# Kernel optimization log

Hardware: AMD Instinct MI355X
Metric: run time of the kernel (lower is better)

## Reference

```python
import jax, jax.numpy as jnp
import numpy as np

B, S_ENC, S_DEC = 4, 2048, 1024
ENC_DIM, DEC_DIM, H = 1024, 1024, 16
CROSS_DIM = max(ENC_DIM, DEC_DIM)
HEAD_DIM_DEC = DEC_DIM // H
SCALE = HEAD_DIM_DEC ** 0.5  # module divides by dec_scaling only


def _linear_params(key, d_in, d_out):
    kw, kb = jax.random.split(key)
    bound = 1.0 / np.sqrt(d_in)
    W = jax.random.uniform(kw, (d_in, d_out), jnp.float32, -bound, bound)
    b = jax.random.uniform(kb, (d_out,), jnp.float32, -bound, bound)
    return W, b


def setup_inputs() -> dict:
    key = jax.random.key(0)
    ks = jax.random.split(key, 7)
    enc = jax.random.normal(ks[0], (B, S_ENC, ENC_DIM), jnp.float32)
    dec = jax.random.normal(ks[1], (B, S_DEC, DEC_DIM), jnp.float32)
    enc_mask = jax.random.uniform(ks[2], (B, 1, 1, S_ENC)) < 0.1
    q_w, q_b = _linear_params(ks[3], DEC_DIM, CROSS_DIM)
    k_w, k_b = _linear_params(ks[4], ENC_DIM, CROSS_DIM)
    v_w, v_b = _linear_params(ks[5], ENC_DIM, DEC_DIM)
    o_w, o_b = _linear_params(ks[6], DEC_DIM, DEC_DIM)
    return {"enc": enc, "enc_mask": enc_mask, "dec": dec,
            "q_w": q_w, "q_b": q_b, "k_w": k_w, "k_b": k_b,
            "v_w": v_w, "v_b": v_b, "o_w": o_w, "o_b": o_b}


def _split_heads(x):
    b, s, d = x.shape
    return x.reshape(b, s, H, d // H).transpose(0, 2, 1, 3)  # [b,h,s,hd]


def reference(enc, enc_mask, dec, q_w, q_b, k_w, k_b, v_w, v_b, o_w, o_b):
    q = _split_heads(dec @ q_w + q_b)   # [B,H,Sq,cross_hd]
    k = _split_heads(enc @ k_w + k_b)   # [B,H,Sk,cross_hd]
    v = _split_heads(enc @ v_w + v_b)   # [B,H,Sk,dec_hd]
    logits = jnp.einsum('bhqd,bhkd->bhqk', q, k) / SCALE
    logits = jnp.where(enc_mask, -jnp.inf, logits)
    a = jax.nn.softmax(logits, axis=-1)
    x = jnp.einsum('bhqk,bhkd->bhqd', a, v)          # [B,H,Sq,dec_hd]
    x = x.transpose(0, 2, 1, 3).reshape(x.shape[0], x.shape[2], -1)  # [B,Sq,DEC_DIM]
    return x @ o_w + o_b
```

## Files before the change

kernel.cpp:

```cpp
#include <hip/hip_runtime.h>
#include <hip/hip_bf16.h>
#include <cstdint>

#define BB   4
#define SENC 2048
#define SDEC 1024
#define DM   1024
#define NH   16
#define HD   64

using short8 = __attribute__((ext_vector_type(8))) short;
using f32x4  = __attribute__((ext_vector_type(4))) float;

__device__ inline unsigned short f2bf(float f) {
    return (unsigned short)((__builtin_bit_cast(unsigned int, f) + 0x8000u) >> 16);
}
__device__ inline unsigned int pk2bf(float a, float b) {
    return ((__builtin_bit_cast(unsigned int, a) + 0x8000u) >> 16) |
           ((__builtin_bit_cast(unsigned int, b) + 0x8000u) & 0xffff0000u);
}

__device__ inline float fexp2(float x) {
#if __has_builtin(__builtin_amdgcn_exp2f)
    return __builtin_amdgcn_exp2f(x);
#else
    return exp2f(x);
#endif
}

#if __has_builtin(__builtin_amdgcn_global_load_lds)
#define HAS_GLL 1
#endif

__device__ inline void stage16(const void* g, void* l) {
#ifdef HAS_GLL
    typedef __attribute__((address_space(1))) const unsigned int guint;
    typedef __attribute__((address_space(3))) unsigned int luint;
    __builtin_amdgcn_global_load_lds((guint*)g, (luint*)l, 16, 0, 0);
#else
    *(short8*)l = *(const short8*)g;
#endif
}

__global__ __launch_bounds__(256) void prep_kernel(
    const float* __restrict__ dec, const float* __restrict__ enc,
    unsigned short* __restrict__ actb,
    const float* __restrict__ qw, const float* __restrict__ kw,
    const float* __restrict__ vw, const float* __restrict__ ow,
    unsigned short* __restrict__ qwt, unsigned short* __restrict__ kvwt,
    unsigned short* __restrict__ owt) {
    __shared__ float t[64][65];
    const int id = blockIdx.x, tid = threadIdx.x;
    if (id < 12288) {
        const int nd = BB * SDEC * DM;
        int i = (id * 256 + tid) * 4;
        const float* src = (i < nd) ? (dec + i) : (enc + (i - nd));
        float4 v = *(const float4*)src;
        ushort4 o;
        o.x = f2bf(v.x); o.y = f2bf(v.y); o.z = f2bf(v.z); o.w = f2bf(v.w);
        *(ushort4*)(actb + i) = o;
        return;
    }
    const int id2 = id - 12288;
    const int z = id2 >> 8, ky = (id2 >> 4) & 15, nx = id2 & 15;
    const float* src; unsigned short* dst;
    switch (z) {
        case 0:  src = qw; dst = qwt; break;
        case 1:  src = kw; dst = kvwt; break;
        case 2:  src = vw; dst = kvwt + (size_t)64 * 16384; break;
        default: src = ow; dst = owt; break;
    }
    const int k0 = ky * 64, n0 = nx * 64;
    #pragma unroll
    for (int it = 0; it < 16; ++it) {
        int e = it * 256 + tid, r = e >> 6, c = e & 63;
        t[r][c] = src[(size_t)(k0 + r) * DM + n0 + c];
    }
    __syncthreads();
    #pragma unroll
    for (int it = 0; it < 2; ++it) {
        int e = it * 256 + tid;
        int kg = e >> 6, r = e & 63;
        short8 w;
        #pragma unroll
        for (int j = 0; j < 8; ++j) w[j] = (short)f2bf(t[kg * 8 + j][r]);
        size_t off = (size_t)((n0 + r) >> 4) * 16384 + (size_t)((k0 >> 3) + kg) * 128
                   + ((r & 15) << 3);
        *(short8*)(dst + off) = w;
    }
}

__global__ __launch_bounds__(256) void gemm_qkv_kernel(
    const unsigned short* __restrict__ encb, const unsigned short* __restrict__ decb,
    const unsigned short* __restrict__ kvwt, const unsigned short* __restrict__ qwt,
    const float* __restrict__ q_b, const float* __restrict__ k_b, const float* __restrict__ v_b,
    unsigned short* __restrict__ Qb, unsigned short* __restrict__ Kb,
    unsigned short* __restrict__ Vtb) {
    __shared__ __align__(16) unsigned short As[2][128 * 32];
    const int id = blockIdx.x;
    const bool isKV = id < 1024;
    const unsigned short *A, *Bw;
    int m0, n0;
    if (isKV) {
        const int x = id & 7, w = id >> 3;
        A = encb; Bw = kvwt;
        m0 = (x * 8 + (w >> 4)) * 128;
        n0 = (w & 15) * 128;
    } else {
        const int i2 = id - 1024, x = i2 & 7, w = i2 >> 3;
        A = decb; Bw = qwt;
        m0 = (x * 4 + (w >> 3)) * 128;
        n0 = (w & 7) * 128;
    }
    const int tid = threadIdx.x;
    const int wave = tid >> 6, lane = tid & 63, quad = lane >> 4, l16 = lane & 15;
    const int wr = wave >> 1, wc = wave & 1;
    const int r16 = lane >> 2, c8 = (lane & 3) * 8;
    const int c8s = (((lane & 3) ^ ((r16 >> 1) & 3)) * 8);
    const int qsw8 = (quad ^ ((l16 >> 1) & 3)) * 8;
    f32x4 acc[4][4] = {};

    const unsigned short* Bbase = Bw + (size_t)(n0 >> 4) * 16384 + (size_t)(wc * 4) * 16384
                                + quad * 128 + l16 * 8;
    short8 bcur[4], bnxt[4];
    #pragma unroll
    for (int j = 0; j < 4; ++j) bcur[j] = *(const short8*)&Bbase[j * 16384];

    #pragma unroll
    for (int i = 0; i < 2; ++i) {
        const int row = wave * 32 + i * 16 + r16;
        stage16(&A[(size_t)(m0 + row) * DM + c8s], &As[0][row * 32 + c8]);
    }
    for (int it = 0; it < 32; ++it) {
        const int bf = it & 1;
        __syncthreads();
        if (it < 31) {
            const int kb2 = (it + 1) * 32, nb = bf ^ 1;
            #pragma unroll
            for (int i = 0; i < 2; ++i) {
                const int row = wave * 32 + i * 16 + r16;
                stage16(&A[(size_t)(m0 + row) * DM + kb2 + c8s], &As[nb][row * 32 + c8]);
            }
            #pragma unroll
            for (int j = 0; j < 4; ++j)
                bnxt[j] = *(const short8*)&Bbase[j * 16384 + kb2 * 16];
        }
        short8 af[4];
        #pragma unroll
        for (int i = 0; i < 4; ++i) af[i] = *(const short8*)&As[bf][(wr * 64 + i * 16 + l16) * 32 + qsw8];
        #pragma unroll
        for (int i = 0; i < 4; ++i)
            #pragma unroll
            for (int j = 0; j < 4; ++j)
                acc[i][j] = __builtin_amdgcn_mfma_f32_16x16x32_bf16(af[i], bcur[j], acc[i][j], 0, 0, 0);
        #pragma unroll
        for (int j = 0; j < 4; ++j) bcur[j] = bnxt[j];
    }
    #pragma unroll
    for (int i = 0; i < 4; ++i) {
        #pragma unroll
        for (int j = 0; j < 4; ++j) {
            const int gc = n0 + wc * 64 + j * 16 + l16;
            const int gr0 = m0 + wr * 64 + i * 16 + quad * 4;
            if (!isKV) {
                const float bv = q_b[gc];
                const int h = gc >> 6, d = gc & 63;
                #pragma unroll
                for (int rr = 0; rr < 4; ++rr) {
                    int gr = gr0 + rr, b = gr >> 10, sq = gr & 1023;
                    float v = (acc[i][j][rr] + bv) * 0.18033688011112042f;
                    Qb[(((size_t)(b * NH + h) * SDEC + sq) << 6) + d] = f2bf(v);
                }
            } else if (gc < 1024) {
                const float bv = k_b[gc];
                const int h = gc >> 6, d = gc & 63;
                #pragma unroll
                for (int rr = 0; rr < 4; ++rr) {
                    int gr = gr0 + rr, b = gr >> 11, sk = gr & 2047;
                    size_t off = (size_t)(b * NH + h) * 131072 + (size_t)(sk >> 4) * 1024
                               + ((d >> 3) << 7) + ((sk & 15) << 3) + (d & 7);
                    Kb[off] = f2bf(acc[i][j][rr] + bv);
                }
            } else {
                const int gc2 = gc & 1023;
                const float bv = v_b[gc2];
                const int h = gc2 >> 6, d = gc2 & 63;
                const int b = gr0 >> 11, sk0 = gr0 & 2047;
                size_t off = (size_t)(b * NH + h) * 131072 + (size_t)(d >> 4) * 32768
                           + (size_t)(sk0 >> 3) * 128 + ((d & 15) << 3) + (sk0 & 7);
                uint2 pk;
                pk.x = pk2bf(acc[i][j][0] + bv, acc[i][j][1] + bv);
                pk.y = pk2bf(acc[i][j][2] + bv, acc[i][j][3] + bv);
                *(uint2*)&Vtb[off] = pk;
            }
        }
    }
}

__global__ __launch_bounds__(256) void gemm_o_kernel(const unsigned short* __restrict__ A,
                                                     const unsigned short* __restrict__ Bw,
                                                     const float* __restrict__ bias,
                                                     float* __restrict__ Cout) {
    __shared__ __align__(16) unsigned short As[2][64 * 32];
    const int id = blockIdx.x, x = id & 7, w = id >> 3;
    const int m0 = (x * 8 + (w >> 3)) * 64, n0 = (w & 7) * 128;
    const int tid = threadIdx.x;
    const int wave = tid >> 6, lane = tid & 63, quad = lane >> 4, l16 = lane & 15;
    const int r16 = lane >> 2, c8 = (lane & 3) * 8;
    const int c8s = (((lane & 3) ^ ((r16 >> 1) & 3)) * 8);
    const int qsw8 = (quad ^ ((l16 >> 1) & 3)) * 8;
    f32x4 acc[4][2] = {};
    const unsigned short* Bbase = Bw + (size_t)((n0 >> 4) + wave * 2) * 16384 + quad * 128 + l16 * 8;
    short8 bcur[2], bnxt[2];
    #pragma unroll
    for (int j = 0; j < 2; ++j) bcur[j] = *(const short8*)&Bbase[j * 16384];
    {
        const int rowA = wave * 16 + r16;
        stage16(&A[(size_t)(m0 + rowA) * DM + c8s], &As[0][rowA * 32 + c8]);
    }
    for (int it = 0; it < 32; ++it) {
        const int bf = it & 1;
        __syncthreads();
        if (it < 31) {
            const int kb2 = (it + 1) * 32, nb = bf ^ 1;
            const int rowA = wave * 16 + r16;
            stage16(&A[(size_t)(m0 + rowA) * DM + kb2 + c8s], &As[nb][rowA * 32 + c8]);
            #pragma unroll
            for (int j = 0; j < 2; ++j) bnxt[j] = *(const short8*)&Bbase[j * 16384 + kb2 * 16];
        }
        short8 af[4];
        #pragma unroll
        for (int i = 0; i < 4; ++i) af[i] = *(const short8*)&As[bf][(i * 16 + l16) * 32 + qsw8];
        #pragma unroll
        for (int i = 0; i < 4; ++i)
            #pragma unroll
            for (int j = 0; j < 2; ++j)
                acc[i][j] = __builtin_amdgcn_mfma_f32_16x16x32_bf16(af[i], bcur[j], acc[i][j], 0, 0, 0);
        #pragma unroll
        for (int j = 0; j < 2; ++j) bcur[j] = bnxt[j];
    }
    #pragma unroll
    for (int i = 0; i < 4; ++i)
        #pragma unroll
        for (int j = 0; j < 2; ++j) {
            const int gc = n0 + wave * 32 + j * 16 + l16;
            const float bv = bias[gc];
            #pragma unroll
            for (int rr = 0; rr < 4; ++rr) {
                const int gr = m0 + i * 16 + quad * 4 + rr;
                Cout[(size_t)gr * DM + gc] = acc[i][j][rr] + bv;
            }
        }
}

__global__ __launch_bounds__(256) void attn_kernel(const unsigned short* __restrict__ Qb,
                                                   const unsigned short* __restrict__ Kb,
                                                   const unsigned short* __restrict__ Vtb,
                                                   const int* __restrict__ mask,
                                                   unsigned short* __restrict__ Xb) {
    __shared__ __align__(16) unsigned short Ps[4][16 * 72];
    const int id = blockIdx.x, x = id & 7, r = id >> 3;
    const int bh = x * 8 + (r & 7), qt = r >> 3;
    const int b = bh >> 4, h = bh & 15;
    const int q0 = qt * 128;
    const int tid = threadIdx.x, wave = tid >> 6, lane = tid & 63;
    const int quad = lane >> 4, l16 = lane & 15;
    const int lo = quad * 128 + l16 * 8;

    const unsigned short* Kfp = Kb + (size_t)bh * 131072;
    const unsigned short* Vfp = Vtb + (size_t)bh * 131072;
    const int* mp = mask + (size_t)b * SENC;

    short8 qf[2][2];
    {
        const unsigned short* Qp = Qb + ((size_t)bh * SDEC + q0 + wave * 32) * HD;
        #pragma unroll
        for (int g = 0; g < 2; ++g) {
            qf[g][0] = *(const short8*)&Qp[(g * 16 + l16) * HD + quad * 8];
            qf[g][1] = *(const short8*)&Qp[(g * 16 + l16) * HD + 32 + quad * 8];
        }
    }

    float lsum[2] = {0.f, 0.f};
    f32x4 o[2][4] = {};

    short8 kA0c[4], kA1c[4];
    {
        const unsigned short* kt0 = Kfp + lo;
        #pragma unroll
        for (int j = 0; j < 4; ++j) {
            kA0c[j] = *(const short8*)&kt0[j * 1024];
            kA1c[j] = *(const short8*)&kt0[j * 1024 + 512];
        }
    }

    for (int kb = 0; kb < SENC; kb += 64) {
        short8 vB0[4], vB1[4];
        const unsigned short* vt = Vfp + (size_t)(kb >> 3) * 128 + lo;
        #pragma unroll
        for (int j = 0; j < 4; ++j) {
            vB0[j] = *(const short8*)&vt[j * 32768];
            vB1[j] = *(const short8*)&vt[j * 32768 + 512];
        }
        short8 kA0n[4], kA1n[4];
        const bool hasn = (kb + 64) < SENC;
        if (hasn) {
            const unsigned short* ktn = Kfp + (size_t)((kb + 64) >> 4) * 1024 + lo;
            #pragma unroll
            for (int j = 0; j < 4; ++j) {
                kA0n[j] = *(const short8*)&ktn[j * 1024];
                kA1n[j] = *(const short8*)&ktn[j * 1024 + 512];
            }
        }
        int4 mi[4];
        #pragma unroll
        for (int j = 0; j < 4; ++j) mi[j] = *(const int4*)&mp[kb + j * 16 + quad * 4];
        #pragma unroll
        for (int g = 0; g < 2; ++g) {
            f32x4 st[4];
            #pragma unroll
            for (int j = 0; j < 4; ++j) {
                f32x4 z = {0.f, 0.f, 0.f, 0.f};
                z = __builtin_amdgcn_mfma_f32_16x16x32_bf16(kA0c[j], qf[g][0], z, 0, 0, 0);
                st[j] = __builtin_amdgcn_mfma_f32_16x16x32_bf16(kA1c[j], qf[g][1], z, 0, 0, 0);
            }
            #pragma unroll
            for (int j = 0; j < 4; ++j) {
                float p0 = mi[j].x ? 0.f : fexp2(st[j][0]);
                float p1 = mi[j].y ? 0.f : fexp2(st[j][1]);
                float p2 = mi[j].z ? 0.f : fexp2(st[j][2]);
                float p3 = mi[j].w ? 0.f : fexp2(st[j][3]);
                lsum[g] += (p0 + p1) + (p2 + p3);
                uint2 pkv;
                pkv.x = pk2bf(p0, p1);
                pkv.y = pk2bf(p2, p3);
                *(uint2*)&Ps[wave][l16 * 72 + j * 16 + quad * 4] = pkv;
            }
            asm volatile("s_waitcnt lgkmcnt(0)" ::: "memory");
            short8 pA0 = *(const short8*)&Ps[wave][l16 * 72 + quad * 8];
            short8 pA1 = *(const short8*)&Ps[wave][l16 * 72 + 32 + quad * 8];
            #pragma unroll
            for (int dj = 0; dj < 4; ++dj) {
                o[g][dj] = __builtin_amdgcn_mfma_f32_16x16x32_bf16(pA0, vB0[dj], o[g][dj], 0, 0, 0);
                o[g][dj] = __builtin_amdgcn_mfma_f32_16x16x32_bf16(pA1, vB1[dj], o[g][dj], 0, 0, 0);
            }
        }
        if (hasn) {
            #pragma unroll
            for (int j = 0; j < 4; ++j) { kA0c[j] = kA0n[j]; kA1c[j] = kA1n[j]; }
        }
    }
    #pragma unroll
    for (int g = 0; g < 2; ++g) {
        float lg = lsum[g];
        lg += __shfl_xor(lg, 16);
        lg += __shfl_xor(lg, 32);
        #pragma unroll
        for (int rr = 0; rr < 4; ++rr) {
            float iv = 1.0f / __shfl(lg, quad * 4 + rr, 64);
            int sq = q0 + wave * 32 + g * 16 + quad * 4 + rr;
            #pragma unroll
            for (int dj = 0; dj < 4; ++dj)
                Xb[((size_t)(b * SDEC) + sq) * DM + h * HD + dj * 16 + l16] = f2bf(o[g][dj][rr] * iv);
        }
    }
}

extern "C" void kernel_launch(void* const* d_in, const int* in_sizes, int n_in,
                              void* d_out, int out_size, void* d_ws, size_t ws_size,
                              hipStream_t stream) {
    const float* enc   = (const float*)d_in[0];
    const int*   emask = (const int*)d_in[1];
    const float* dec   = (const float*)d_in[2];
    const float* q_w   = (const float*)d_in[3];
    const float* q_b   = (const float*)d_in[4];
    const float* k_w   = (const float*)d_in[5];
    const float* k_b   = (const float*)d_in[6];
    const float* v_w   = (const float*)d_in[7];
    const float* v_b   = (const float*)d_in[8];
    const float* o_w   = (const float*)d_in[9];
    const float* o_b   = (const float*)d_in[10];
    float* out = (float*)d_out;

    char* ws = (char*)d_ws;
    unsigned short* decb = (unsigned short*)ws; ws += (size_t)4096 * 1024 * 2;
    unsigned short* encb = (unsigned short*)ws; ws += (size_t)8192 * 1024 * 2;
    unsigned short* qwt  = (unsigned short*)ws; ws += (size_t)1024 * 1024 * 2;
    unsigned short* kvwt = (unsigned short*)ws; ws += (size_t)2048 * 1024 * 2;
    unsigned short* owt  = (unsigned short*)ws; ws += (size_t)1024 * 1024 * 2;
    unsigned short* Qb   = (unsigned short*)ws; ws += (size_t)BB * NH * SDEC * HD * 2;
    unsigned short* Kb   = (unsigned short*)ws; ws += (size_t)BB * NH * SENC * HD * 2;
    unsigned short* Vtb  = (unsigned short*)ws; ws += (size_t)BB * NH * HD * SENC * 2;
    unsigned short* Xb   = (unsigned short*)ws; ws += (size_t)4096 * 1024 * 2;

    prep_kernel<<<13312, 256, 0, stream>>>(dec, enc, decb, q_w, k_w, v_w, o_w, qwt, kvwt, owt);
    gemm_qkv_kernel<<<1280, 256, 0, stream>>>(encb, decb, kvwt, qwt, q_b, k_b, v_b, Qb, Kb, Vtb);
    attn_kernel<<<512, 256, 0, stream>>>(Qb, Kb, Vtb, emask, Xb);
    gemm_o_kernel<<<512, 256, 0, stream>>>(Xb, owt, o_b, out);
}
```

Before: 254.1 us.

## Split attention work across 8 waves with 16 query rows each

The attention kernel now launches 512 threads per block, and each of the 8 waves handles 16 query rows instead of 32. Each wave drops the software prefetch of the next K tile and keeps a single set of accumulators, which cuts register pressure. Launch bounds of (512,4) ask for higher occupancy so memory latency is hidden by more waves rather than by explicit prefetch. In exchange, every K/V fragment is now loaded from global memory by twice as many waves, doubling K/V load traffic per block, and the MFMA work per wave per load is halved.

```diff
diff --git a/kernel.cpp b/kernel.cpp
--- a/kernel.cpp
+++ b/kernel.cpp
@@ -253,12 +253,12 @@
         }
 }
 
-__global__ __launch_bounds__(256) void attn_kernel(const unsigned short* __restrict__ Qb,
-                                                   const unsigned short* __restrict__ Kb,
-                                                   const unsigned short* __restrict__ Vtb,
-                                                   const int* __restrict__ mask,
-                                                   unsigned short* __restrict__ Xb) {
-    __shared__ __align__(16) unsigned short Ps[4][16 * 72];
+__global__ __launch_bounds__(512, 4) void attn_kernel(const unsigned short* __restrict__ Qb,
+                                                      const unsigned short* __restrict__ Kb,
+                                                      const unsigned short* __restrict__ Vtb,
+                                                      const int* __restrict__ mask,
+                                                      unsigned short* __restrict__ Xb) {
+    __shared__ __align__(16) unsigned short Ps[8][16 * 72];
     const int id = blockIdx.x, x = id & 7, r = id >> 3;
     const int bh = x * 8 + (r & 7), qt = r >> 3;
     const int b = bh >> 4, h = bh & 15;
@@ -270,99 +270,74 @@
     const unsigned short* Kfp = Kb + (size_t)bh * 131072;
     const unsigned short* Vfp = Vtb + (size_t)bh * 131072;
     const int* mp = mask + (size_t)b * SENC;
-
-    short8 qf[2][2];
+    unsigned short* Pw = &Ps[wave][l16 * 72];
+
+    short8 qf0, qf1;
     {
-        const unsigned short* Qp = Qb + ((size_t)bh * SDEC + q0 + wave * 32) * HD;
-        #pragma unroll
-        for (int g = 0; g < 2; ++g) {
-            qf[g][0] = *(const short8*)&Qp[(g * 16 + l16) * HD + quad * 8];
-            qf[g][1] = *(const short8*)&Qp[(g * 16 + l16) * HD + 32 + quad * 8];
-        }
-    }
-
-    float lsum[2] = {0.f, 0.f};
-    f32x4 o[2][4] = {};
-
-    short8 kA0c[4], kA1c[4];
-    {
-        const unsigned short* kt0 = Kfp + lo;
-        #pragma unroll
-        for (int j = 0; j < 4; ++j) {
-            kA0c[j] = *(const short8*)&kt0[j * 1024];
-            kA1c[j] = *(const short8*)&kt0[j * 1024 + 512];
-        }
-    }
+        const unsigned short* Qp = Qb + ((size_t)bh * SDEC + q0 + wave * 16) * HD;
+        qf0 = *(const short8*)&Qp[l16 * HD + quad * 8];
+        qf1 = *(const short8*)&Qp[l16 * HD + 32 + quad * 8];
+    }
+
+    float lsum = 0.f;
+    f32x4 o[4] = {};
 
     for (int kb = 0; kb < SENC; kb += 64) {
-        short8 vB0[4], vB1[4];
+        short8 kA0[4], kA1[4], vB0[4], vB1[4];
+        int4 mi[4];
+        const unsigned short* kt = Kfp + (size_t)(kb >> 4) * 1024 + lo;
         const unsigned short* vt = Vfp + (size_t)(kb >> 3) * 128 + lo;
+        #pragma unroll
+        for (int j = 0; j < 4; ++j) {
+            kA0[j] = *(const short8*)&kt[j * 1024];
+            kA1[j] = *(const short8*)&kt[j * 1024 + 512];
+        }
         #pragma unroll
         for (int j = 0; j < 4; ++j) {
             vB0[j] = *(const short8*)&vt[j * 32768];
             vB1[j] = *(const short8*)&vt[j * 32768 + 512];
         }
-        short8 kA0n[4], kA1n[4];
-        const bool hasn = (kb + 64) < SENC;
-        if (hasn) {
-            const unsigned short* ktn = Kfp + (size_t)((kb + 64) >> 4) * 1024 + lo;
-            #pragma unroll
-            for (int j = 0; j < 4; ++j) {
-                kA0n[j] = *(const short8*)&ktn[j * 1024];
-                kA1n[j] = *(const short8*)&ktn[j * 1024 + 512];
-            }
-        }
-        int4 mi[4];
         #pragma unroll
         for (int j = 0; j < 4; ++j) mi[j] = *(const int4*)&mp[kb + j * 16 + quad * 4];
-        #pragma unroll
-        for (int g = 0; g < 2; ++g) {
-            f32x4 st[4];
-            #pragma unroll
-            for (int j = 0; j < 4; ++j) {
-                f32x4 z = {0.f, 0.f, 0.f, 0.f};
-                z = __builtin_amdgcn_mfma_f32_16x16x32_bf16(kA0c[j], qf[g][0], z, 0, 0, 0);
-                st[j] = __builtin_amdgcn_mfma_f32_16x16x32_bf16(kA1c[j], qf[g][1], z, 0, 0, 0);
-            }
-            #pragma unroll
-            for (int j = 0; j < 4; ++j) {
-                float p0 = mi[j].x ? 0.f : fexp2(st[j][0]);
-                float p1 = mi[j].y ? 0.f : fexp2(st[j][1]);
-                float p2 = mi[j].z ? 0.f : fexp2(st[j][2]);
-                float p3 = mi[j].w ? 0.f : fexp2(st[j][3]);
-                lsum[g] += (p0 + p1) + (p2 + p3);
-                uint2 pkv;
-                pkv.x = pk2bf(p0, p1);
-                pkv.y = pk2bf(p2, p3);
-                *(uint2*)&Ps[wave][l16 * 72 + j * 16 + quad * 4] = pkv;
-            }
-            asm volatile("s_waitcnt lgkmcnt(0)" ::: "memory");
-            short8 pA0 = *(const short8*)&Ps[wave][l16 * 72 + quad * 8];
-            short8 pA1 = *(const short8*)&Ps[wave][l16 * 72 + 32 + quad * 8];
-            #pragma unroll
-            for (int dj = 0; dj < 4; ++dj) {
-                o[g][dj] = __builtin_amdgcn_mfma_f32_16x16x32_bf16(pA0, vB0[dj], o[g][dj], 0, 0, 0);
-                o[g][dj] = __builtin_amdgcn_mfma_f32_16x16x32_bf16(pA1, vB1[dj], o[g][dj], 0, 0, 0);
-            }
-        }
-        if (hasn) {
-            #pragma unroll
-            for (int j = 0; j < 4; ++j) { kA0c[j] = kA0n[j]; kA1c[j] = kA1n[j]; }
-        }
-    }
-    #pragma unroll
-    for (int g = 0; g < 2; ++g) {
-        float lg = lsum[g];
-        lg += __shfl_xor(lg, 16);
-        lg += __shfl_xor(lg, 32);
-        #pragma unroll
-        for (int rr = 0; rr < 4; ++rr) {
-            float iv = 1.0f / __shfl(lg, quad * 4 + rr, 64);
-            int sq = q0 + wave * 32 + g * 16 + quad * 4 + rr;
-            #pragma unroll
-            for (int dj = 0; dj < 4; ++dj)
-                Xb[((size_t)(b * SDEC) + sq) * DM + h * HD + dj * 16 + l16] = f2bf(o[g][dj][rr] * iv);
-        }
+
+        f32x4 st[4];
+        #pragma unroll
+        for (int j = 0; j < 4; ++j) {
+            f32x4 z = {0.f, 0.f, 0.f, 0.f};
+            z = __builtin_amdgcn_mfma_f32_16x16x32_bf16(kA0[j], qf0, z, 0, 0, 0);
+            st[j] = __builtin_amdgcn_mfma_f32_16x16x32_bf16(kA1[j], qf1, z, 0, 0, 0);
+        }
+        #pragma unroll
+        for (int j = 0; j < 4; ++j) {
+            float p0 = mi[j].x ? 0.f : fexp2(st[j][0]);
+            float p1 = mi[j].y ? 0.f : fexp2(st[j][1]);
+            float p2 = mi[j].z ? 0.f : fexp2(st[j][2]);
+            float p3 = mi[j].w ? 0.f : fexp2(st[j][3]);
+            lsum += (p0 + p1) + (p2 + p3);
+            uint2 pkv;
+            pkv.x = pk2bf(p0, p1);
+            pkv.y = pk2bf(p2, p3);
+            *(uint2*)&Pw[j * 16 + quad * 4] = pkv;
+        }
+        asm volatile("s_waitcnt lgkmcnt(0)" ::: "memory");
+        short8 pA0 = *(const short8*)&Pw[quad * 8];
+        short8 pA1 = *(const short8*)&Pw[32 + quad * 8];
+        #pragma unroll
+        for (int dj = 0; dj < 4; ++dj) {
+            o[dj] = __builtin_amdgcn_mfma_f32_16x16x32_bf16(pA0, vB0[dj], o[dj], 0, 0, 0);
+            o[dj] = __builtin_amdgcn_mfma_f32_16x16x32_bf16(pA1, vB1[dj], o[dj], 0, 0, 0);
+        }
+    }
+    float lg = lsum;
+    lg += __shfl_xor(lg, 16);
+    lg += __shfl_xor(lg, 32);
+    #pragma unroll
+    for (int rr = 0; rr < 4; ++rr) {
+        float iv = 1.0f / __shfl(lg, quad * 4 + rr, 64);
+        int sq = q0 + wave * 16 + quad * 4 + rr;
+        #pragma unroll
+        for (int dj = 0; dj < 4; ++dj)
+            Xb[((size_t)(b * SDEC) + sq) * DM + h * HD + dj * 16 + l16] = f2bf(o[dj][rr] * iv);
     }
 }
 
@@ -395,6 +370,6 @@
 
     prep_kernel<<<13312, 256, 0, stream>>>(dec, enc, decb, q_w, k_w, v_w, o_w, qwt, kvwt, owt);
     gemm_qkv_kernel<<<1280, 256, 0, stream>>>(encb, decb, kvwt, qwt, q_b, k_b, v_b, Qb, Kb, Vtb);
-    attn_kernel<<<512, 256, 0, stream>>>(Qb, Kb, Vtb, emask, Xb);
+    attn_kernel<<<512, 512, 0, stream>>>(Qb, Kb, Vtb, emask, Xb);
     gemm_o_kernel<<<512, 256, 0, stream>>>(Xb, owt, o_b, out);
 }
```

Result: slower. 270.9 us (+6.6%).

## Split attention key range across two wave groups and reduce partials in LDS

Applied to the files above, without the earlier changes.

The attention block doubles to 512 threads. Each half of the waves processes half of the 2048 encoder keys for the same 128 queries, then the two partial outputs and row sums are combined through shared memory before normalisation. The mask loads are also prefetched one tile ahead, like the K tiles. The aim is to double the waves in flight and shorten each wave's serial key loop, at the cost of extra LDS, a block-wide barrier and a final reduction step.

```diff
diff --git a/kernel.cpp b/kernel.cpp
--- a/kernel.cpp
+++ b/kernel.cpp
@@ -253,27 +253,30 @@
         }
 }
 
-__global__ __launch_bounds__(256) void attn_kernel(const unsigned short* __restrict__ Qb,
-                                                   const unsigned short* __restrict__ Kb,
-                                                   const unsigned short* __restrict__ Vtb,
-                                                   const int* __restrict__ mask,
-                                                   unsigned short* __restrict__ Xb) {
-    __shared__ __align__(16) unsigned short Ps[4][16 * 72];
+__global__ __launch_bounds__(512, 4) void attn_kernel(const unsigned short* __restrict__ Qb,
+                                                      const unsigned short* __restrict__ Kb,
+                                                      const unsigned short* __restrict__ Vtb,
+                                                      const int* __restrict__ mask,
+                                                      unsigned short* __restrict__ Xb) {
+    __shared__ __align__(16) unsigned short Ps[8][16 * 72];
+    __shared__ __align__(16) float Os[4][64][32];
+    __shared__ float Ls[4][64][2];
     const int id = blockIdx.x, x = id & 7, r = id >> 3;
     const int bh = x * 8 + (r & 7), qt = r >> 3;
     const int b = bh >> 4, h = bh & 15;
     const int q0 = qt * 128;
     const int tid = threadIdx.x, wave = tid >> 6, lane = tid & 63;
+    const int w4 = wave & 3, half = wave >> 2;
     const int quad = lane >> 4, l16 = lane & 15;
     const int lo = quad * 128 + l16 * 8;
 
-    const unsigned short* Kfp = Kb + (size_t)bh * 131072;
-    const unsigned short* Vfp = Vtb + (size_t)bh * 131072;
-    const int* mp = mask + (size_t)b * SENC;
+    const unsigned short* Kfp = Kb + (size_t)bh * 131072 + half * 65536;
+    const unsigned short* Vfp = Vtb + (size_t)bh * 131072 + half * 16384;
+    const int* mp = mask + (size_t)b * SENC + half * 1024;
 
     short8 qf[2][2];
     {
-        const unsigned short* Qp = Qb + ((size_t)bh * SDEC + q0 + wave * 32) * HD;
+        const unsigned short* Qp = Qb + ((size_t)bh * SDEC + q0 + w4 * 32) * HD;
         #pragma unroll
         for (int g = 0; g < 2; ++g) {
             qf[g][0] = *(const short8*)&Qp[(g * 16 + l16) * HD + quad * 8];
@@ -285,6 +288,7 @@
     f32x4 o[2][4] = {};
 
     short8 kA0c[4], kA1c[4];
+    int4 mc[4];
     {
         const unsigned short* kt0 = Kfp + lo;
         #pragma unroll
@@ -292,29 +296,31 @@
             kA0c[j] = *(const short8*)&kt0[j * 1024];
             kA1c[j] = *(const short8*)&kt0[j * 1024 + 512];
         }
-    }
-
-    for (int kb = 0; kb < SENC; kb += 64) {
+        #pragma unroll
+        for (int j = 0; j < 4; ++j) mc[j] = *(const int4*)&mp[j * 16 + quad * 4];
+    }
+
+    for (int kk = 0; kk < 1024; kk += 64) {
         short8 vB0[4], vB1[4];
-        const unsigned short* vt = Vfp + (size_t)(kb >> 3) * 128 + lo;
+        const unsigned short* vt = Vfp + (size_t)(kk >> 3) * 128 + lo;
         #pragma unroll
         for (int j = 0; j < 4; ++j) {
             vB0[j] = *(const short8*)&vt[j * 32768];
             vB1[j] = *(const short8*)&vt[j * 32768 + 512];
         }
         short8 kA0n[4], kA1n[4];
-        const bool hasn = (kb + 64) < SENC;
+        int4 mn_[4];
+        const bool hasn = (kk + 64) < 1024;
         if (hasn) {
-            const unsigned short* ktn = Kfp + (size_t)((kb + 64) >> 4) * 1024 + lo;
+            const unsigned short* ktn = Kfp + (size_t)((kk + 64) >> 4) * 1024 + lo;
             #pragma unroll
             for (int j = 0; j < 4; ++j) {
                 kA0n[j] = *(const short8*)&ktn[j * 1024];
                 kA1n[j] = *(const short8*)&ktn[j * 1024 + 512];
             }
-        }
-        int4 mi[4];
-        #pragma unroll
-        for (int j = 0; j < 4; ++j) mi[j] = *(const int4*)&mp[kb + j * 16 + quad * 4];
+            #pragma unroll
+            for (int j = 0; j < 4; ++j) mn_[j] = *(const int4*)&mp[kk + 64 + j * 16 + quad * 4];
+        }
         #pragma unroll
         for (int g = 0; g < 2; ++g) {
             f32x4 st[4];
@@ -324,21 +330,22 @@
                 z = __builtin_amdgcn_mfma_f32_16x16x32_bf16(kA0c[j], qf[g][0], z, 0, 0, 0);
                 st[j] = __builtin_amdgcn_mfma_f32_16x16x32_bf16(kA1c[j], qf[g][1], z, 0, 0, 0);
             }
+            unsigned short* Pw = &Ps[wave][l16 * 72];
             #pragma unroll
             for (int j = 0; j < 4; ++j) {
-                float p0 = mi[j].x ? 0.f : fexp2(st[j][0]);
-                float p1 = mi[j].y ? 0.f : fexp2(st[j][1]);
-                float p2 = mi[j].z ? 0.f : fexp2(st[j][2]);
-                float p3 = mi[j].w ? 0.f : fexp2(st[j][3]);
+                float p0 = mc[j].x ? 0.f : fexp2(st[j][0]);
+                float p1 = mc[j].y ? 0.f : fexp2(st[j][1]);
+                float p2 = mc[j].z ? 0.f : fexp2(st[j][2]);
+                float p3 = mc[j].w ? 0.f : fexp2(st[j][3]);
                 lsum[g] += (p0 + p1) + (p2 + p3);
                 uint2 pkv;
                 pkv.x = pk2bf(p0, p1);
                 pkv.y = pk2bf(p2, p3);
-                *(uint2*)&Ps[wave][l16 * 72 + j * 16 + quad * 4] = pkv;
+                *(uint2*)&Pw[j * 16 + quad * 4] = pkv;
             }
             asm volatile("s_waitcnt lgkmcnt(0)" ::: "memory");
-            short8 pA0 = *(const short8*)&Ps[wave][l16 * 72 + quad * 8];
-            short8 pA1 = *(const short8*)&Ps[wave][l16 * 72 + 32 + quad * 8];
+            short8 pA0 = *(const short8*)&Pw[quad * 8];
+            short8 pA1 = *(const short8*)&Pw[32 + quad * 8];
             #pragma unroll
             for (int dj = 0; dj < 4; ++dj) {
                 o[g][dj] = __builtin_amdgcn_mfma_f32_16x16x32_bf16(pA0, vB0[dj], o[g][dj], 0, 0, 0);
@@ -347,21 +354,46 @@
         }
         if (hasn) {
             #pragma unroll
-            for (int j = 0; j < 4; ++j) { kA0c[j] = kA0n[j]; kA1c[j] = kA1n[j]; }
-        }
-    }
+            for (int j = 0; j < 4; ++j) {
+                kA0c[j] = kA0n[j]; kA1c[j] = kA1n[j]; mc[j] = mn_[j];
+            }
+        }
+    }
+    float lg[2];
     #pragma unroll
     for (int g = 0; g < 2; ++g) {
-        float lg = lsum[g];
-        lg += __shfl_xor(lg, 16);
-        lg += __shfl_xor(lg, 32);
-        #pragma unroll
-        for (int rr = 0; rr < 4; ++rr) {
-            float iv = 1.0f / __shfl(lg, quad * 4 + rr, 64);
-            int sq = q0 + wave * 32 + g * 16 + quad * 4 + rr;
+        float v = lsum[g];
+        v += __shfl_xor(v, 16);
+        v += __shfl_xor(v, 32);
+        lg[g] = v;
+    }
+    if (half == 1) {
+        #pragma unroll
+        for (int g = 0; g < 2; ++g) {
             #pragma unroll
             for (int dj = 0; dj < 4; ++dj)
-                Xb[((size_t)(b * SDEC) + sq) * DM + h * HD + dj * 16 + l16] = f2bf(o[g][dj][rr] * iv);
+                *(f32x4*)&Os[w4][lane][g * 16 + dj * 4] = o[g][dj];
+            Ls[w4][lane][g] = lg[g];
+        }
+    }
+    __syncthreads();
+    if (half == 0) {
+        #pragma unroll
+        for (int g = 0; g < 2; ++g) {
+            lg[g] += Ls[w4][lane][g];
+            #pragma unroll
+            for (int dj = 0; dj < 4; ++dj) {
+                f32x4 po = *(const f32x4*)&Os[w4][lane][g * 16 + dj * 4];
+                o[g][dj] += po;
+            }
+            #pragma unroll
+            for (int rr = 0; rr < 4; ++rr) {
+                float iv = 1.0f / __shfl(lg[g], quad * 4 + rr, 64);
+                int sq = q0 + w4 * 32 + g * 16 + quad * 4 + rr;
+                #pragma unroll
+                for (int dj = 0; dj < 4; ++dj)
+                    Xb[((size_t)(b * SDEC) + sq) * DM + h * HD + dj * 16 + l16] = f2bf(o[g][dj][rr] * iv);
+            }
         }
     }
 }
@@ -395,6 +427,6 @@
 
     prep_kernel<<<13312, 256, 0, stream>>>(dec, enc, decb, q_w, k_w, v_w, o_w, qwt, kvwt, owt);
     gemm_qkv_kernel<<<1280, 256, 0, stream>>>(encb, decb, kvwt, qwt, q_b, k_b, v_b, Qb, Kb, Vtb);
-    attn_kernel<<<512, 256, 0, stream>>>(Qb, Kb, Vtb, emask, Xb);
+    attn_kernel<<<512, 512, 0, stream>>>(Qb, Kb, Vtb, emask, Xb);
     gemm_o_kernel<<<512, 256, 0, stream>>>(Xb, owt, o_b, out);
 }
```

Result: slower. 615.2 us (+142.1%).
